# Performance work log

Measured on AMD Instinct MI355X. Metric: run time of the kernel, lower is better.

The kernel has to match this reference:

```python
import jax, jax.numpy as jnp
import numpy as np

N_NODES = 100000
N_EDGES = 1250000
IN_DIM = 128
HID_DIM = 64
OUT_DIM = 16


def setup_inputs() -> dict:
    key = jax.random.key(0)
    k1, k2, k3, k4, k5, k6, k7 = jax.random.split(key, 7)
    x = jax.random.normal(k1, (N_NODES, IN_DIM), dtype=jnp.float32)
    edge_index = jax.random.randint(k2, (2, N_EDGES), 0, N_NODES, dtype=jnp.int64)
    s = 1.0 / np.sqrt(IN_DIM)
    W1 = jax.random.uniform(k3, (IN_DIM, HID_DIM), jnp.float32, -s, s)
    b1 = jax.random.uniform(k4, (HID_DIM,), jnp.float32, -s, s)
    s2 = 1.0 / np.sqrt(HID_DIM)
    W2 = jax.random.uniform(k5, (HID_DIM, OUT_DIM), jnp.float32, -s2, s2)
    b2 = jax.random.uniform(k6, (OUT_DIM,), jnp.float32, -s2, s2)
    return {"x": x, "edge_index": edge_index, "W1": W1, "b1": b1, "W2": W2, "b2": b2}


def reference(x, edge_index, W1, b1, W2, b2):
    # GCNConv (PyG default): linear transform, add self-loops, symmetric norm,
    # gather-scatter aggregation, bias. Then relu -> linear -> log_softmax.
    N = x.shape[0]
    loop = jnp.arange(N, dtype=edge_index.dtype)
    src = jnp.concatenate([edge_index[0], loop])  # message sources
    dst = jnpp_concat = jnp.concatenate([edge_index[1], loop])  # message targets
    # degree (with self-loops) computed on destination nodes
    deg = jax.ops.segment_sum(jnp.ones_like(dst, dtype=x.dtype), dst, num_segments=N)
    deg_inv_sqrt = jnp.where(deg > 0, jax.lax.rsqrt(deg), 0.0)
    norm = deg_inv_sqrt[src] * deg_inv_sqrt[dst]  # [E+N]
    h = x @ W1  # [N, hid] -- transform before aggregation (fewer bytes moved)
    msg = h[src] * norm[:, None]  # gather: [E+N, hid]
    agg = jax.ops.segment_sum(msg, dst, num_segments=N) + b1  # scatter-add
    h = jax.nn.relu(agg)
    logits = h @ W2 + b2
    return jax.nn.log_softmax(logits, axis=-1)
```

## Files before the change

kernel.cpp:

```cpp
#include <hip/hip_runtime.h>
#include <hip/hip_bf16.h>

#define N_NODES 100000
#define N_EDGES 1250000
#define IN_DIM  128
#define HID     64
#define OUTD    16
#define ROW     64
#define NRANGE  8
#define RSIZE   12500
#define NCHUNK  128
#define CHUNK   9768
#define FILLB   (NRANGE * NCHUNK)
#define MTILE   128
#define GEMMB   ((N_NODES + MTILE - 1) / MTILE)

typedef __attribute__((ext_vector_type(8))) short  short8;
typedef __attribute__((ext_vector_type(4))) float  floatx4;
typedef __attribute__((ext_vector_type(4))) float  f32x4;
typedef __attribute__((ext_vector_type(4))) int    i32x4;

__device__ __forceinline__ unsigned short f2bf(float f) {
    unsigned u = __float_as_uint(f);
    u += 0x7fffu + ((u >> 16) & 1u);
    return (unsigned short)(u >> 16);
}
__device__ __forceinline__ unsigned pk2(float lo, float hi) {
    __hip_bfloat162 t = __float22bfloat162_rn(make_float2(lo, hi));
    return *reinterpret_cast<unsigned*>(&t);
}
__device__ __forceinline__ float bf2f_lo(unsigned u) { return __uint_as_float(u << 16); }
__device__ __forceinline__ float bf2f_hi(unsigned u) { return __uint_as_float(u & 0xffff0000u); }

__global__ __launch_bounds__(256) void zero_cursor(int* __restrict__ cursor,
                                                   unsigned* __restrict__ hb_dummy) {
    int i = blockIdx.x * 256 + threadIdx.x;
    if (i < N_NODES) cursor[i] = 0;
    if (i < 32) hb_dummy[i] = 0u;
}

__global__ __launch_bounds__(256) void fill_gemm(const float* __restrict__ x,
                                                 const float* __restrict__ W1,
                                                 const int* __restrict__ src,
                                                 const int* __restrict__ dst,
                                                 int* __restrict__ cursor,
                                                 int* __restrict__ csr,
                                                 unsigned short* __restrict__ hb) {
    __shared__ unsigned short w1t[HID][132];

    if (blockIdx.x < FILLB) {
        const int r  = blockIdx.x & 7;
        const int c  = blockIdx.x >> 3;
        const int lo = r * RSIZE;
        const int q1 = min(N_EDGES, (c + 1) * CHUNK) >> 2;
        for (int q = (c * CHUNK >> 2) + threadIdx.x; q < q1; q += 256) {
            i32x4 d4 = __builtin_nontemporal_load(((const i32x4*)dst) + q);
            i32x4 s4 = __builtin_nontemporal_load(((const i32x4*)src) + q);
#pragma unroll
            for (int u = 0; u < 4; u++) {
                int d = (u == 0) ? d4.x : (u == 1) ? d4.y : (u == 2) ? d4.z : d4.w;
                int s = (u == 0) ? s4.x : (u == 1) ? s4.y : (u == 2) ? s4.z : s4.w;
                if ((unsigned)(d - lo) < (unsigned)RSIZE) {
                    int p = atomicAdd(&cursor[d], 1);
                    if (p < ROW) csr[(size_t)d * ROW + p] = s;
                }
            }
        }
        return;
    }

    const int m0 = (blockIdx.x - FILLB) * MTILE;

    for (int q = threadIdx.x; q < IN_DIM * HID / 4; q += 256) {
        int k = q >> 4, n = (q & 15) * 4;
        float4 wq = ((const float4*)W1)[q];
        w1t[n + 0][k] = f2bf(wq.x);
        w1t[n + 1][k] = f2bf(wq.y);
        w1t[n + 2][k] = f2bf(wq.z);
        w1t[n + 3][k] = f2bf(wq.w);
    }
    __syncthreads();

    const int lane = threadIdx.x & 63;
    const int w    = threadIdx.x >> 6;
    const int mrow = lane & 15;
    const int quad = lane >> 4;
    const int rowa = min(m0 + w * 32 + mrow,      N_NODES - 1);
    const int rowb = min(m0 + w * 32 + 16 + mrow, N_NODES - 1);

    floatx4 acc[2][4] = {};
#pragma unroll
    for (int k0 = 0; k0 < IN_DIM; k0 += 32) {
        union { unsigned u[4]; short8 s; } a0, a1;
        {
            const f32x4* pa = (const f32x4*)(x + (size_t)rowa * IN_DIM + k0 + quad * 8);
            f32x4 u0 = __builtin_nontemporal_load(pa);
            f32x4 v0 = __builtin_nontemporal_load(pa + 1);
            a0.u[0] = pk2(u0.x, u0.y); a0.u[1] = pk2(u0.z, u0.w);
            a0.u[2] = pk2(v0.x, v0.y); a0.u[3] = pk2(v0.z, v0.w);
            const f32x4* pb = (const f32x4*)(x + (size_t)rowb * IN_DIM + k0 + quad * 8);
            f32x4 u1 = __builtin_nontemporal_load(pb);
            f32x4 v1 = __builtin_nontemporal_load(pb + 1);
            a1.u[0] = pk2(u1.x, u1.y); a1.u[1] = pk2(u1.z, u1.w);
            a1.u[2] = pk2(v1.x, v1.y); a1.u[3] = pk2(v1.z, v1.w);
        }
        short8 b0 = *(const short8*)&w1t[ 0 + mrow][k0 + quad * 8];
        short8 b1 = *(const short8*)&w1t[16 + mrow][k0 + quad * 8];
        short8 b2 = *(const short8*)&w1t[32 + mrow][k0 + quad * 8];
        short8 b3 = *(const short8*)&w1t[48 + mrow][k0 + quad * 8];
        acc[0][0] = __builtin_amdgcn_mfma_f32_16x16x32_bf16(a0.s, b0, acc[0][0], 0, 0, 0);
        acc[0][1] = __builtin_amdgcn_mfma_f32_16x16x32_bf16(a0.s, b1, acc[0][1], 0, 0, 0);
        acc[0][2] = __builtin_amdgcn_mfma_f32_16x16x32_bf16(a0.s, b2, acc[0][2], 0, 0, 0);
        acc[0][3] = __builtin_amdgcn_mfma_f32_16x16x32_bf16(a0.s, b3, acc[0][3], 0, 0, 0);
        acc[1][0] = __builtin_amdgcn_mfma_f32_16x16x32_bf16(a1.s, b0, acc[1][0], 0, 0, 0);
        acc[1][1] = __builtin_amdgcn_mfma_f32_16x16x32_bf16(a1.s, b1, acc[1][1], 0, 0, 0);
        acc[1][2] = __builtin_amdgcn_mfma_f32_16x16x32_bf16(a1.s, b2, acc[1][2], 0, 0, 0);
        acc[1][3] = __builtin_amdgcn_mfma_f32_16x16x32_bf16(a1.s, b3, acc[1][3], 0, 0, 0);
    }

#pragma unroll
    for (int tm = 0; tm < 2; tm++) {
#pragma unroll
        for (int reg = 0; reg < 4; reg++) {
            int m = m0 + w * 32 + tm * 16 + quad * 4 + reg;
            if (m < N_NODES) {
#pragma unroll
                for (int tn = 0; tn < 4; tn++)
                    __builtin_nontemporal_store(f2bf(acc[tm][tn][reg]),
                                                &hb[(size_t)m * HID + tn * 16 + mrow]);
            }
        }
    }
}

__global__ __launch_bounds__(256) void pull_epilogue(const unsigned short* __restrict__ hb,
                                                     const int* __restrict__ csr,
                                                     const int* __restrict__ deg,
                                                     const float* __restrict__ b1,
                                                     const float* __restrict__ W2,
                                                     const float* __restrict__ b2,
                                                     float* __restrict__ out) {
    const int i     = blockIdx.x * 4 + (threadIdx.x >> 6);
    const int lane  = threadIdx.x & 63;
    const int e_sub = lane >> 4;
    const int f4    = lane & 15;

    const int   dg  = deg[i];
    const int   cnt = min(dg, ROW - 1);
    const float di  = rsqrtf((float)dg + 1.0f);

    int   s_l = N_NODES;
    float w_l = 0.f;
    if (lane < cnt) {
        s_l = __builtin_nontemporal_load(csr + (size_t)i * ROW + lane);
        w_l = rsqrtf((float)deg[s_l] + 1.0f);
    } else if (lane == cnt) {
        s_l = i;
        w_l = di;
    }

    const uint2* hbv = (const uint2*)hb + f4;

    float ax = 0.f, ay = 0.f, az = 0.f, aw = 0.f;
    const int R = (cnt + 16) >> 4;
    for (int r = 0; r < R; ++r) {
        const int e0 = (r << 4) + e_sub;
        int   s0 = __shfl(s_l, e0,      64), s1 = __shfl(s_l, e0 + 4,  64);
        int   s2 = __shfl(s_l, e0 + 8,  64), s3 = __shfl(s_l, e0 + 12, 64);
        float w0 = __shfl(w_l, e0,      64), w1 = __shfl(w_l, e0 + 4,  64);
        float w2 = __shfl(w_l, e0 + 8,  64), w3 = __shfl(w_l, e0 + 12, 64);
        uint2 a = hbv[s0 << 4];
        uint2 b = hbv[s1 << 4];
        uint2 c = hbv[s2 << 4];
        uint2 d = hbv[s3 << 4];
        ax = fmaf(bf2f_lo(a.x), w0, ax); ay = fmaf(bf2f_hi(a.x), w0, ay);
        az = fmaf(bf2f_lo(a.y), w0, az); aw = fmaf(bf2f_hi(a.y), w0, aw);
        ax = fmaf(bf2f_lo(b.x), w1, ax); ay = fmaf(bf2f_hi(b.x), w1, ay);
        az = fmaf(bf2f_lo(b.y), w1, az); aw = fmaf(bf2f_hi(b.y), w1, aw);
        ax = fmaf(bf2f_lo(c.x), w2, ax); ay = fmaf(bf2f_hi(c.x), w2, ay);
        az = fmaf(bf2f_lo(c.y), w2, az); aw = fmaf(bf2f_hi(c.y), w2, aw);
        ax = fmaf(bf2f_lo(d.x), w3, ax); ay = fmaf(bf2f_hi(d.x), w3, ay);
        az = fmaf(bf2f_lo(d.y), w3, az); aw = fmaf(bf2f_hi(d.y), w3, aw);
    }

    ax += __shfl_xor(ax, 16, 64); ax += __shfl_xor(ax, 32, 64);
    ay += __shfl_xor(ay, 16, 64); ay += __shfl_xor(ay, 32, 64);
    az += __shfl_xor(az, 16, 64); az += __shfl_xor(az, 32, 64);
    aw += __shfl_xor(aw, 16, 64); aw += __shfl_xor(aw, 32, 64);

    float4 b1v = ((const float4*)b1)[f4];
    float v0 = fmaxf(fmaf(ax, di, b1v.x), 0.f);
    float v1 = fmaxf(fmaf(ay, di, b1v.y), 0.f);
    float v2 = fmaxf(fmaf(az, di, b1v.z), 0.f);
    float v3 = fmaxf(fmaf(aw, di, b1v.w), 0.f);

    const float4* W2v = (const float4*)W2;
    float4 w0 = W2v[(4 * f4 + 0) * 4 + e_sub];
    float4 w1 = W2v[(4 * f4 + 1) * 4 + e_sub];
    float4 w2 = W2v[(4 * f4 + 2) * 4 + e_sub];
    float4 w3 = W2v[(4 * f4 + 3) * 4 + e_sub];
    float p0 = v0 * w0.x + v1 * w1.x + v2 * w2.x + v3 * w3.x;
    float p1 = v0 * w0.y + v1 * w1.y + v2 * w2.y + v3 * w3.y;
    float p2 = v0 * w0.z + v1 * w1.z + v2 * w2.z + v3 * w3.z;
    float p3 = v0 * w0.w + v1 * w1.w + v2 * w2.w + v3 * w3.w;
#pragma unroll
    for (int d = 1; d < 16; d <<= 1) {
        p0 += __shfl_xor(p0, d, 64);
        p1 += __shfl_xor(p1, d, 64);
        p2 += __shfl_xor(p2, d, 64);
        p3 += __shfl_xor(p3, d, 64);
    }
    float4 b2v = ((const float4*)b2)[e_sub];
    float lg0 = p0 + b2v.x, lg1 = p1 + b2v.y, lg2 = p2 + b2v.z, lg3 = p3 + b2v.w;

    float m = fmaxf(fmaxf(lg0, lg1), fmaxf(lg2, lg3));
    m = fmaxf(m, __shfl_xor(m, 16, 64));
    m = fmaxf(m, __shfl_xor(m, 32, 64));
    float s = __expf(lg0 - m) + __expf(lg1 - m) + __expf(lg2 - m) + __expf(lg3 - m);
    s += __shfl_xor(s, 16, 64);
    s += __shfl_xor(s, 32, 64);
    float lse = __logf(s) + m;

    if (f4 == 0) {
        f32x4 o = {lg0 - lse, lg1 - lse, lg2 - lse, lg3 - lse};
        __builtin_nontemporal_store(o, ((f32x4*)out) + (size_t)i * 4 + e_sub);
    }
}

extern "C" void kernel_launch(void* const* d_in, const int* in_sizes, int n_in,
                              void* d_out, int out_size, void* d_ws, size_t ws_size,
                              hipStream_t stream) {
    const float* x   = (const float*)d_in[0];
    const int*   ei  = (const int*)d_in[1];
    const float* W1  = (const float*)d_in[2];
    const float* b1  = (const float*)d_in[3];
    const float* W2  = (const float*)d_in[4];
    const float* b2  = (const float*)d_in[5];
    float*       out = (float*)d_out;

    const int* src = ei;
    const int* dst = ei + N_EDGES;

    char* ws = (char*)d_ws;
    size_t off = 0;
    unsigned short* hb = (unsigned short*)(ws + off);
    off += (size_t)(N_NODES + 1) * HID * 2;
    int*   csr    = (int*)  (ws + off); off += ((size_t)N_NODES * ROW + ROW) * 4;
    int*   cursor = (int*)  (ws + off); off += (size_t)N_NODES * 4;

    zero_cursor<<<(N_NODES + 255) / 256, 256, 0, stream>>>(
        cursor, (unsigned*)(hb + (size_t)N_NODES * HID));
    fill_gemm<<<FILLB + GEMMB, 256, 0, stream>>>(x, W1, src, dst, cursor, csr, hb);
    pull_epilogue<<<N_NODES / 4, 256, 0, stream>>>(hb, csr, cursor, b1, W2, b2, out);
}
```

Before: 237.5 us.

## Fuse fill/GEMM and pull stages into one cooperative persistent kernel

Merges the CSR fill + GEMM phase and the pull/epilogue phase into one cooperative kernel with a grid-wide sync, using persistent blocks that loop over tasks and nodes. The zero-init kernel is replaced by hipMemsetAsync calls, and W2/b1/b2 loads are hoisted out of the per-node loop. The aim is to remove kernel launch gaps and per-block setup. The costs are the grid sync, a grid limited to co-resident blocks (capped at 2048), and a possible loss of load balance; a non-cooperative two-kernel fallback is kept.

```diff
diff --git a/kernel.cpp b/kernel.cpp
--- a/kernel.cpp
+++ b/kernel.cpp
@@ -1,5 +1,8 @@
 #include <hip/hip_runtime.h>
 #include <hip/hip_bf16.h>
+#include <hip/hip_cooperative_groups.h>
+
+namespace cg = cooperative_groups;
 
 #define N_NODES 100000
 #define N_EDGES 1250000
@@ -14,6 +17,7 @@
 #define FILLB   (NRANGE * NCHUNK)
 #define MTILE   128
 #define GEMMB   ((N_NODES + MTILE - 1) / MTILE)
+#define NTASK   (FILLB + GEMMB)
 
 typedef __attribute__((ext_vector_type(8))) short  short8;
 typedef __attribute__((ext_vector_type(4))) float  floatx4;
@@ -32,45 +36,38 @@
 __device__ __forceinline__ float bf2f_lo(unsigned u) { return __uint_as_float(u << 16); }
 __device__ __forceinline__ float bf2f_hi(unsigned u) { return __uint_as_float(u & 0xffff0000u); }
 
-__global__ __launch_bounds__(256) void zero_cursor(int* __restrict__ cursor,
-                                                   unsigned* __restrict__ hb_dummy) {
-    int i = blockIdx.x * 256 + threadIdx.x;
-    if (i < N_NODES) cursor[i] = 0;
-    if (i < 32) hb_dummy[i] = 0u;
-}
-
-__global__ __launch_bounds__(256) void fill_gemm(const float* __restrict__ x,
-                                                 const float* __restrict__ W1,
-                                                 const int* __restrict__ src,
-                                                 const int* __restrict__ dst,
-                                                 int* __restrict__ cursor,
-                                                 int* __restrict__ csr,
-                                                 unsigned short* __restrict__ hb) {
-    __shared__ unsigned short w1t[HID][132];
-
-    if (blockIdx.x < FILLB) {
-        const int r  = blockIdx.x & 7;
-        const int c  = blockIdx.x >> 3;
-        const int lo = r * RSIZE;
-        const int q1 = min(N_EDGES, (c + 1) * CHUNK) >> 2;
-        for (int q = (c * CHUNK >> 2) + threadIdx.x; q < q1; q += 256) {
-            i32x4 d4 = __builtin_nontemporal_load(((const i32x4*)dst) + q);
-            i32x4 s4 = __builtin_nontemporal_load(((const i32x4*)src) + q);
-#pragma unroll
-            for (int u = 0; u < 4; u++) {
-                int d = (u == 0) ? d4.x : (u == 1) ? d4.y : (u == 2) ? d4.z : d4.w;
-                int s = (u == 0) ? s4.x : (u == 1) ? s4.y : (u == 2) ? s4.z : s4.w;
-                if ((unsigned)(d - lo) < (unsigned)RSIZE) {
-                    int p = atomicAdd(&cursor[d], 1);
-                    if (p < ROW) csr[(size_t)d * ROW + p] = s;
-                }
+__device__ __forceinline__ void fill_task(int task, const int* __restrict__ src,
+                                          const int* __restrict__ dst,
+                                          int* __restrict__ cursor,
+                                          int* __restrict__ csr) {
+    const int r  = task & 7;
+    const int c  = task >> 3;
+    const int lo = r * RSIZE;
+    const int q1 = min(N_EDGES, (c + 1) * CHUNK) >> 2;
+    for (int q = (c * CHUNK >> 2) + threadIdx.x; q < q1; q += 256) {
+        i32x4 d4 = __builtin_nontemporal_load(((const i32x4*)dst) + q);
+        i32x4 s4 = __builtin_nontemporal_load(((const i32x4*)src) + q);
+#pragma unroll
+        for (int u = 0; u < 4; u++) {
+            int d = (u == 0) ? d4.x : (u == 1) ? d4.y : (u == 2) ? d4.z : d4.w;
+            int s = (u == 0) ? s4.x : (u == 1) ? s4.y : (u == 2) ? s4.z : s4.w;
+            if ((unsigned)(d - lo) < (unsigned)RSIZE) {
+                int p = atomicAdd(&cursor[d], 1);
+                if (p < ROW) csr[(size_t)d * ROW + p] = s;
             }
         }
-        return;
-    }
-
-    const int m0 = (blockIdx.x - FILLB) * MTILE;
-
+    }
+}
+
+__device__ __forceinline__ void gemm_task(int task, unsigned short (*w1t)[132],
+                                          const float* __restrict__ x,
+                                          const float* __restrict__ W1,
+                                          unsigned short* __restrict__ hb) {
+    const int m0 = (task - FILLB) * MTILE;
+    const int lane = threadIdx.x & 63;
+    const int w    = threadIdx.x >> 6;
+
+    __syncthreads();
     for (int q = threadIdx.x; q < IN_DIM * HID / 4; q += 256) {
         int k = q >> 4, n = (q & 15) * 4;
         float4 wq = ((const float4*)W1)[q];
@@ -81,8 +78,6 @@
     }
     __syncthreads();
 
-    const int lane = threadIdx.x & 63;
-    const int w    = threadIdx.x >> 6;
     const int mrow = lane & 15;
     const int quad = lane >> 4;
     const int rowa = min(m0 + w * 32 + mrow,      N_NODES - 1);
@@ -133,17 +128,16 @@
     }
 }
 
-__global__ __launch_bounds__(256) void pull_epilogue(const unsigned short* __restrict__ hb,
-                                                     const int* __restrict__ csr,
-                                                     const int* __restrict__ deg,
-                                                     const float* __restrict__ b1,
-                                                     const float* __restrict__ W2,
-                                                     const float* __restrict__ b2,
-                                                     float* __restrict__ out) {
-    const int i     = blockIdx.x * 4 + (threadIdx.x >> 6);
+__device__ __forceinline__ void pull_node(int i, const unsigned short* __restrict__ hb,
+                                          const int* __restrict__ csr,
+                                          const int* __restrict__ deg,
+                                          float4 b1v, float4 w2r0, float4 w2r1,
+                                          float4 w2r2, float4 w2r3, float4 b2v,
+                                          float* __restrict__ out) {
     const int lane  = threadIdx.x & 63;
     const int e_sub = lane >> 4;
     const int f4    = lane & 15;
+    const uint2* hbv = (const uint2*)hb + f4;
 
     const int   dg  = deg[i];
     const int   cnt = min(dg, ROW - 1);
@@ -158,8 +152,6 @@
         s_l = i;
         w_l = di;
     }
-
-    const uint2* hbv = (const uint2*)hb + f4;
 
     float ax = 0.f, ay = 0.f, az = 0.f, aw = 0.f;
     const int R = (cnt + 16) >> 4;
@@ -188,21 +180,15 @@
     az += __shfl_xor(az, 16, 64); az += __shfl_xor(az, 32, 64);
     aw += __shfl_xor(aw, 16, 64); aw += __shfl_xor(aw, 32, 64);
 
-    float4 b1v = ((const float4*)b1)[f4];
     float v0 = fmaxf(fmaf(ax, di, b1v.x), 0.f);
     float v1 = fmaxf(fmaf(ay, di, b1v.y), 0.f);
     float v2 = fmaxf(fmaf(az, di, b1v.z), 0.f);
     float v3 = fmaxf(fmaf(aw, di, b1v.w), 0.f);
 
-    const float4* W2v = (const float4*)W2;
-    float4 w0 = W2v[(4 * f4 + 0) * 4 + e_sub];
-    float4 w1 = W2v[(4 * f4 + 1) * 4 + e_sub];
-    float4 w2 = W2v[(4 * f4 + 2) * 4 + e_sub];
-    float4 w3 = W2v[(4 * f4 + 3) * 4 + e_sub];
-    float p0 = v0 * w0.x + v1 * w1.x + v2 * w2.x + v3 * w3.x;
-    float p1 = v0 * w0.y + v1 * w1.y + v2 * w2.y + v3 * w3.y;
-    float p2 = v0 * w0.z + v1 * w1.z + v2 * w2.z + v3 * w3.z;
-    float p3 = v0 * w0.w + v1 * w1.w + v2 * w2.w + v3 * w3.w;
+    float p0 = v0 * w2r0.x + v1 * w2r1.x + v2 * w2r2.x + v3 * w2r3.x;
+    float p1 = v0 * w2r0.y + v1 * w2r1.y + v2 * w2r2.y + v3 * w2r3.y;
+    float p2 = v0 * w2r0.z + v1 * w2r1.z + v2 * w2r2.z + v3 * w2r3.z;
+    float p3 = v0 * w2r0.w + v1 * w2r1.w + v2 * w2r2.w + v3 * w2r3.w;
 #pragma unroll
     for (int d = 1; d < 16; d <<= 1) {
         p0 += __shfl_xor(p0, d, 64);
@@ -210,7 +196,6 @@
         p2 += __shfl_xor(p2, d, 64);
         p3 += __shfl_xor(p3, d, 64);
     }
-    float4 b2v = ((const float4*)b2)[e_sub];
     float lg0 = p0 + b2v.x, lg1 = p1 + b2v.y, lg2 = p2 + b2v.z, lg3 = p3 + b2v.w;
 
     float m = fmaxf(fmaxf(lg0, lg1), fmaxf(lg2, lg3));
@@ -225,6 +210,78 @@
         f32x4 o = {lg0 - lse, lg1 - lse, lg2 - lse, lg3 - lse};
         __builtin_nontemporal_store(o, ((f32x4*)out) + (size_t)i * 4 + e_sub);
     }
+}
+
+__global__ __launch_bounds__(256) void fused(const float* __restrict__ x,
+                                             const float* __restrict__ W1,
+                                             const int* __restrict__ src,
+                                             const int* __restrict__ dst,
+                                             int* __restrict__ cursor,
+                                             int* __restrict__ csr,
+                                             unsigned short* __restrict__ hb,
+                                             const float* __restrict__ b1,
+                                             const float* __restrict__ W2,
+                                             const float* __restrict__ b2,
+                                             float* __restrict__ out) {
+    __shared__ unsigned short w1t[HID][132];
+
+    for (int task = blockIdx.x; task < NTASK; task += gridDim.x) {
+        if (task < FILLB) fill_task(task, src, dst, cursor, csr);
+        else              gemm_task(task, w1t, x, W1, hb);
+    }
+
+    cg::this_grid().sync();
+
+    const int lane  = threadIdx.x & 63;
+    const int w     = threadIdx.x >> 6;
+    const int e_sub = lane >> 4;
+    const int f4    = lane & 15;
+    const int* deg  = cursor;
+
+    const float4  b1v = ((const float4*)b1)[f4];
+    const float4* W2v = (const float4*)W2;
+    const float4  w2r0 = W2v[(4 * f4 + 0) * 4 + e_sub];
+    const float4  w2r1 = W2v[(4 * f4 + 1) * 4 + e_sub];
+    const float4  w2r2 = W2v[(4 * f4 + 2) * 4 + e_sub];
+    const float4  w2r3 = W2v[(4 * f4 + 3) * 4 + e_sub];
+    const float4  b2v = ((const float4*)b2)[e_sub];
+
+    const int nw = gridDim.x * 4;
+    for (int i = blockIdx.x * 4 + w; i < N_NODES; i += nw)
+        pull_node(i, hb, csr, deg, b1v, w2r0, w2r1, w2r2, w2r3, b2v, out);
+}
+
+__global__ __launch_bounds__(256) void fill_gemm_k(const float* __restrict__ x,
+                                                   const float* __restrict__ W1,
+                                                   const int* __restrict__ src,
+                                                   const int* __restrict__ dst,
+                                                   int* __restrict__ cursor,
+                                                   int* __restrict__ csr,
+                                                   unsigned short* __restrict__ hb) {
+    __shared__ unsigned short w1t[HID][132];
+    if (blockIdx.x < FILLB) fill_task(blockIdx.x, src, dst, cursor, csr);
+    else                    gemm_task(blockIdx.x, w1t, x, W1, hb);
+}
+
+__global__ __launch_bounds__(256) void pull_k(const unsigned short* __restrict__ hb,
+                                              const int* __restrict__ csr,
+                                              const int* __restrict__ deg,
+                                              const float* __restrict__ b1,
+                                              const float* __restrict__ W2,
+                                              const float* __restrict__ b2,
+                                              float* __restrict__ out) {
+    const int lane  = threadIdx.x & 63;
+    const int e_sub = lane >> 4;
+    const int f4    = lane & 15;
+    const float4  b1v = ((const float4*)b1)[f4];
+    const float4* W2v = (const float4*)W2;
+    const float4  w2r0 = W2v[(4 * f4 + 0) * 4 + e_sub];
+    const float4  w2r1 = W2v[(4 * f4 + 1) * 4 + e_sub];
+    const float4  w2r2 = W2v[(4 * f4 + 2) * 4 + e_sub];
+    const float4  w2r3 = W2v[(4 * f4 + 3) * 4 + e_sub];
+    const float4  b2v = ((const float4*)b2)[e_sub];
+    const int i = blockIdx.x * 4 + (threadIdx.x >> 6);
+    pull_node(i, hb, csr, deg, b1v, w2r0, w2r1, w2r2, w2r3, b2v, out);
 }
 
 extern "C" void kernel_launch(void* const* d_in, const int* in_sizes, int n_in,
@@ -248,8 +305,37 @@
     int*   csr    = (int*)  (ws + off); off += ((size_t)N_NODES * ROW + ROW) * 4;
     int*   cursor = (int*)  (ws + off); off += (size_t)N_NODES * 4;
 
-    zero_cursor<<<(N_NODES + 255) / 256, 256, 0, stream>>>(
-        cursor, (unsigned*)(hb + (size_t)N_NODES * HID));
-    fill_gemm<<<FILLB + GEMMB, 256, 0, stream>>>(x, W1, src, dst, cursor, csr, hb);
-    pull_epilogue<<<N_NODES / 4, 256, 0, stream>>>(hb, csr, cursor, b1, W2, b2, out);
-}
+    static int coopGrid = -2;
+    if (coopGrid == -2) {
+        int bpc = 0, ncu = 256;
+        hipDeviceProp_t prop;
+        if (hipGetDeviceProperties(&prop, 0) == hipSuccess) ncu = prop.multiProcessorCount;
+        if (hipOccupancyMaxActiveBlocksPerMultiprocessor(&bpc, (const void*)fused, 256, 0)
+                == hipSuccess && bpc >= 1) {
+            int g = bpc * ncu;
+            if (g > 2048) g = 2048;
+            g &= ~7;
+            coopGrid = (g >= 8) ? g : -1;
+        } else {
+            coopGrid = -1;
+        }
+    }
+
+    hipMemsetAsync(cursor, 0, (size_t)N_NODES * 4, stream);
+    hipMemsetAsync(hb + (size_t)N_NODES * HID, 0, HID * sizeof(unsigned short), stream);
+
+    bool done = false;
+    if (coopGrid > 0) {
+        void* args[] = {(void*)&x, (void*)&W1, (void*)&src, (void*)&dst,
+                        (void*)&cursor, (void*)&csr, (void*)&hb,
+                        (void*)&b1, (void*)&W2, (void*)&b2, (void*)&out};
+        hipError_t e = hipLaunchCooperativeKernel((const void*)fused, dim3(coopGrid),
+                                                  dim3(256), args, 0, stream);
+        if (e == hipSuccess) done = true;
+        else coopGrid = -1;
+    }
+    if (!done) {
+        fill_gemm_k<<<FILLB + GEMMB, 256, 0, stream>>>(x, W1, src, dst, cursor, csr, hb);
+        pull_k<<<N_NODES / 4, 256, 0, stream>>>(hb, csr, cursor, b1, W2, b2, out);
+    }
+}
```

New measurement: 376.8 us. 1.59x slower.

## Process four nodes per wavefront in pull epilogue and batch fill atomics

Applied to the files above, without the earlier changes.

The pull/epilogue kernel now gives each wavefront four destination nodes and interleaves their gathers, so more independent loads are in flight per wave and the W2/b1/b2 loads are shared. The fill phase issues its four atomics before the dependent CSR stores and uses twice as many, smaller chunks. The zeroing kernel is replaced by hipMemsetAsync, and padding source lanes now point at node 0 with weight 0 instead of a zeroed dummy row. This trades more registers and less wave-level parallelism in the epilogue for memory-level parallelism.

```diff
diff --git a/kernel.cpp b/kernel.cpp
--- a/kernel.cpp
+++ b/kernel.cpp
@@ -9,11 +9,12 @@
 #define ROW     64
 #define NRANGE  8
 #define RSIZE   12500
-#define NCHUNK  128
-#define CHUNK   9768
+#define NCHUNK  256
+#define CHUNK   4888
 #define FILLB   (NRANGE * NCHUNK)
 #define MTILE   128
 #define GEMMB   ((N_NODES + MTILE - 1) / MTILE)
+#define NPW     4
 
 typedef __attribute__((ext_vector_type(8))) short  short8;
 typedef __attribute__((ext_vector_type(4))) float  floatx4;
@@ -31,13 +32,6 @@
 }
 __device__ __forceinline__ float bf2f_lo(unsigned u) { return __uint_as_float(u << 16); }
 __device__ __forceinline__ float bf2f_hi(unsigned u) { return __uint_as_float(u & 0xffff0000u); }
-
-__global__ __launch_bounds__(256) void zero_cursor(int* __restrict__ cursor,
-                                                   unsigned* __restrict__ hb_dummy) {
-    int i = blockIdx.x * 256 + threadIdx.x;
-    if (i < N_NODES) cursor[i] = 0;
-    if (i < 32) hb_dummy[i] = 0u;
-}
 
 __global__ __launch_bounds__(256) void fill_gemm(const float* __restrict__ x,
                                                  const float* __restrict__ W1,
@@ -56,15 +50,19 @@
         for (int q = (c * CHUNK >> 2) + threadIdx.x; q < q1; q += 256) {
             i32x4 d4 = __builtin_nontemporal_load(((const i32x4*)dst) + q);
             i32x4 s4 = __builtin_nontemporal_load(((const i32x4*)src) + q);
-#pragma unroll
-            for (int u = 0; u < 4; u++) {
-                int d = (u == 0) ? d4.x : (u == 1) ? d4.y : (u == 2) ? d4.z : d4.w;
-                int s = (u == 0) ? s4.x : (u == 1) ? s4.y : (u == 2) ? s4.z : s4.w;
-                if ((unsigned)(d - lo) < (unsigned)RSIZE) {
-                    int p = atomicAdd(&cursor[d], 1);
-                    if (p < ROW) csr[(size_t)d * ROW + p] = s;
-                }
-            }
+            int p0 = 0, p1 = 0, p2 = 0, p3 = 0;
+            const bool k0 = (unsigned)(d4.x - lo) < (unsigned)RSIZE;
+            const bool k1 = (unsigned)(d4.y - lo) < (unsigned)RSIZE;
+            const bool k2 = (unsigned)(d4.z - lo) < (unsigned)RSIZE;
+            const bool k3 = (unsigned)(d4.w - lo) < (unsigned)RSIZE;
+            if (k0) p0 = atomicAdd(&cursor[d4.x], 1);
+            if (k1) p1 = atomicAdd(&cursor[d4.y], 1);
+            if (k2) p2 = atomicAdd(&cursor[d4.z], 1);
+            if (k3) p3 = atomicAdd(&cursor[d4.w], 1);
+            if (k0 && p0 < ROW) csr[(size_t)d4.x * ROW + p0] = s4.x;
+            if (k1 && p1 < ROW) csr[(size_t)d4.y * ROW + p1] = s4.y;
+            if (k2 && p2 < ROW) csr[(size_t)d4.z * ROW + p2] = s4.z;
+            if (k3 && p3 < ROW) csr[(size_t)d4.w * ROW + p3] = s4.w;
         }
         return;
     }
@@ -140,90 +138,143 @@
                                                      const float* __restrict__ W2,
                                                      const float* __restrict__ b2,
                                                      float* __restrict__ out) {
-    const int i     = blockIdx.x * 4 + (threadIdx.x >> 6);
     const int lane  = threadIdx.x & 63;
     const int e_sub = lane >> 4;
     const int f4    = lane & 15;
-
-    const int   dg  = deg[i];
-    const int   cnt = min(dg, ROW - 1);
-    const float di  = rsqrtf((float)dg + 1.0f);
-
-    int   s_l = N_NODES;
-    float w_l = 0.f;
-    if (lane < cnt) {
-        s_l = __builtin_nontemporal_load(csr + (size_t)i * ROW + lane);
-        w_l = rsqrtf((float)deg[s_l] + 1.0f);
-    } else if (lane == cnt) {
-        s_l = i;
-        w_l = di;
+    const int base  = blockIdx.x * (4 * NPW) + (threadIdx.x >> 6) * NPW;
+
+    int   dg[NPW], cnt[NPW];
+    float di[NPW];
+#pragma unroll
+    for (int n = 0; n < NPW; n++) {
+        dg[n]  = deg[base + n];
+        cnt[n] = min(dg[n], ROW - 1);
+        di[n]  = rsqrtf((float)dg[n] + 1.0f);
+    }
+
+    int sv[NPW];
+#pragma unroll
+    for (int n = 0; n < NPW; n++) {
+        sv[n] = 0;
+        if (lane < cnt[n])
+            sv[n] = __builtin_nontemporal_load(csr + (size_t)(base + n) * ROW + lane);
+    }
+    float wv[NPW];
+#pragma unroll
+    for (int n = 0; n < NPW; n++) {
+        wv[n] = 0.f;
+        if (lane < cnt[n])       wv[n] = rsqrtf((float)deg[sv[n]] + 1.0f);
+        else if (lane == cnt[n]) { sv[n] = base + n; wv[n] = di[n]; }
     }
 
     const uint2* hbv = (const uint2*)hb + f4;
 
-    float ax = 0.f, ay = 0.f, az = 0.f, aw = 0.f;
-    const int R = (cnt + 16) >> 4;
+    float ax[NPW], ay[NPW], az[NPW], aw[NPW];
+    int   Rn[NPW];
+    int   R = 0;
+#pragma unroll
+    for (int n = 0; n < NPW; n++) {
+        ax[n] = ay[n] = az[n] = aw[n] = 0.f;
+        Rn[n] = (cnt[n] + 16) >> 4;
+        R = max(R, Rn[n]);
+    }
+
     for (int r = 0; r < R; ++r) {
         const int e0 = (r << 4) + e_sub;
-        int   s0 = __shfl(s_l, e0,      64), s1 = __shfl(s_l, e0 + 4,  64);
-        int   s2 = __shfl(s_l, e0 + 8,  64), s3 = __shfl(s_l, e0 + 12, 64);
-        float w0 = __shfl(w_l, e0,      64), w1 = __shfl(w_l, e0 + 4,  64);
-        float w2 = __shfl(w_l, e0 + 8,  64), w3 = __shfl(w_l, e0 + 12, 64);
-        uint2 a = hbv[s0 << 4];
-        uint2 b = hbv[s1 << 4];
-        uint2 c = hbv[s2 << 4];
-        uint2 d = hbv[s3 << 4];
-        ax = fmaf(bf2f_lo(a.x), w0, ax); ay = fmaf(bf2f_hi(a.x), w0, ay);
-        az = fmaf(bf2f_lo(a.y), w0, az); aw = fmaf(bf2f_hi(a.y), w0, aw);
-        ax = fmaf(bf2f_lo(b.x), w1, ax); ay = fmaf(bf2f_hi(b.x), w1, ay);
-        az = fmaf(bf2f_lo(b.y), w1, az); aw = fmaf(bf2f_hi(b.y), w1, aw);
-        ax = fmaf(bf2f_lo(c.x), w2, ax); ay = fmaf(bf2f_hi(c.x), w2, ay);
-        az = fmaf(bf2f_lo(c.y), w2, az); aw = fmaf(bf2f_hi(c.y), w2, aw);
-        ax = fmaf(bf2f_lo(d.x), w3, ax); ay = fmaf(bf2f_hi(d.x), w3, ay);
-        az = fmaf(bf2f_lo(d.y), w3, az); aw = fmaf(bf2f_hi(d.y), w3, aw);
-    }
-
-    ax += __shfl_xor(ax, 16, 64); ax += __shfl_xor(ax, 32, 64);
-    ay += __shfl_xor(ay, 16, 64); ay += __shfl_xor(ay, 32, 64);
-    az += __shfl_xor(az, 16, 64); az += __shfl_xor(az, 32, 64);
-    aw += __shfl_xor(aw, 16, 64); aw += __shfl_xor(aw, 32, 64);
-
-    float4 b1v = ((const float4*)b1)[f4];
-    float v0 = fmaxf(fmaf(ax, di, b1v.x), 0.f);
-    float v1 = fmaxf(fmaf(ay, di, b1v.y), 0.f);
-    float v2 = fmaxf(fmaf(az, di, b1v.z), 0.f);
-    float v3 = fmaxf(fmaf(aw, di, b1v.w), 0.f);
+#pragma unroll
+        for (int n = 0; n < NPW; n++) {
+            if (r < Rn[n]) {
+                int   s0 = __shfl(sv[n], e0,      64), s1 = __shfl(sv[n], e0 + 4,  64);
+                int   s2 = __shfl(sv[n], e0 + 8,  64), s3 = __shfl(sv[n], e0 + 12, 64);
+                float w0 = __shfl(wv[n], e0,      64), w1 = __shfl(wv[n], e0 + 4,  64);
+                float w2 = __shfl(wv[n], e0 + 8,  64), w3 = __shfl(wv[n], e0 + 12, 64);
+                uint2 a = hbv[s0 << 4];
+                uint2 b = hbv[s1 << 4];
+                uint2 c = hbv[s2 << 4];
+                uint2 d = hbv[s3 << 4];
+                ax[n] = fmaf(bf2f_lo(a.x), w0, ax[n]); ay[n] = fmaf(bf2f_hi(a.x), w0, ay[n]);
+                az[n] = fmaf(bf2f_lo(a.y), w0, az[n]); aw[n] = fmaf(bf2f_hi(a.y), w0, aw[n]);
+                ax[n] = fmaf(bf2f_lo(b.x), w1, ax[n]); ay[n] = fmaf(bf2f_hi(b.x), w1, ay[n]);
+                az[n] = fmaf(bf2f_lo(b.y), w1, az[n]); aw[n] = fmaf(bf2f_hi(b.y), w1, aw[n]);
+                ax[n] = fmaf(bf2f_lo(c.x), w2, ax[n]); ay[n] = fmaf(bf2f_hi(c.x), w2, ay[n]);
+                az[n] = fmaf(bf2f_lo(c.y), w2, az[n]); aw[n] = fmaf(bf2f_hi(c.y), w2, aw[n]);
+                ax[n] = fmaf(bf2f_lo(d.x), w3, ax[n]); ay[n] = fmaf(bf2f_hi(d.x), w3, ay[n]);
+                az[n] = fmaf(bf2f_lo(d.y), w3, az[n]); aw[n] = fmaf(bf2f_hi(d.y), w3, aw[n]);
+            }
+        }
+    }
+
+#pragma unroll
+    for (int n = 0; n < NPW; n++) {
+        ax[n] += __shfl_xor(ax[n], 16, 64); ay[n] += __shfl_xor(ay[n], 16, 64);
+        az[n] += __shfl_xor(az[n], 16, 64); aw[n] += __shfl_xor(aw[n], 16, 64);
+    }
+#pragma unroll
+    for (int n = 0; n < NPW; n++) {
+        ax[n] += __shfl_xor(ax[n], 32, 64); ay[n] += __shfl_xor(ay[n], 32, 64);
+        az[n] += __shfl_xor(az[n], 32, 64); aw[n] += __shfl_xor(aw[n], 32, 64);
+    }
+
+    const float4 b1v = ((const float4*)b1)[f4];
+    float4 v[NPW];
+#pragma unroll
+    for (int n = 0; n < NPW; n++) {
+        v[n].x = fmaxf(fmaf(ax[n], di[n], b1v.x), 0.f);
+        v[n].y = fmaxf(fmaf(ay[n], di[n], b1v.y), 0.f);
+        v[n].z = fmaxf(fmaf(az[n], di[n], b1v.z), 0.f);
+        v[n].w = fmaxf(fmaf(aw[n], di[n], b1v.w), 0.f);
+    }
 
     const float4* W2v = (const float4*)W2;
-    float4 w0 = W2v[(4 * f4 + 0) * 4 + e_sub];
-    float4 w1 = W2v[(4 * f4 + 1) * 4 + e_sub];
-    float4 w2 = W2v[(4 * f4 + 2) * 4 + e_sub];
-    float4 w3 = W2v[(4 * f4 + 3) * 4 + e_sub];
-    float p0 = v0 * w0.x + v1 * w1.x + v2 * w2.x + v3 * w3.x;
-    float p1 = v0 * w0.y + v1 * w1.y + v2 * w2.y + v3 * w3.y;
-    float p2 = v0 * w0.z + v1 * w1.z + v2 * w2.z + v3 * w3.z;
-    float p3 = v0 * w0.w + v1 * w1.w + v2 * w2.w + v3 * w3.w;
+    const float4 w2r0 = W2v[(4 * f4 + 0) * 4 + e_sub];
+    const float4 w2r1 = W2v[(4 * f4 + 1) * 4 + e_sub];
+    const float4 w2r2 = W2v[(4 * f4 + 2) * 4 + e_sub];
+    const float4 w2r3 = W2v[(4 * f4 + 3) * 4 + e_sub];
+    float4 p[NPW];
+#pragma unroll
+    for (int n = 0; n < NPW; n++) {
+        p[n].x = v[n].x * w2r0.x + v[n].y * w2r1.x + v[n].z * w2r2.x + v[n].w * w2r3.x;
+        p[n].y = v[n].x * w2r0.y + v[n].y * w2r1.y + v[n].z * w2r2.y + v[n].w * w2r3.y;
+        p[n].z = v[n].x * w2r0.z + v[n].y * w2r1.z + v[n].z * w2r2.z + v[n].w * w2r3.z;
+        p[n].w = v[n].x * w2r0.w + v[n].y * w2r1.w + v[n].z * w2r2.w + v[n].w * w2r3.w;
+    }
 #pragma unroll
     for (int d = 1; d < 16; d <<= 1) {
-        p0 += __shfl_xor(p0, d, 64);
-        p1 += __shfl_xor(p1, d, 64);
-        p2 += __shfl_xor(p2, d, 64);
-        p3 += __shfl_xor(p3, d, 64);
-    }
-    float4 b2v = ((const float4*)b2)[e_sub];
-    float lg0 = p0 + b2v.x, lg1 = p1 + b2v.y, lg2 = p2 + b2v.z, lg3 = p3 + b2v.w;
-
-    float m = fmaxf(fmaxf(lg0, lg1), fmaxf(lg2, lg3));
-    m = fmaxf(m, __shfl_xor(m, 16, 64));
-    m = fmaxf(m, __shfl_xor(m, 32, 64));
-    float s = __expf(lg0 - m) + __expf(lg1 - m) + __expf(lg2 - m) + __expf(lg3 - m);
-    s += __shfl_xor(s, 16, 64);
-    s += __shfl_xor(s, 32, 64);
-    float lse = __logf(s) + m;
+#pragma unroll
+        for (int n = 0; n < NPW; n++) {
+            p[n].x += __shfl_xor(p[n].x, d, 64);
+            p[n].y += __shfl_xor(p[n].y, d, 64);
+            p[n].z += __shfl_xor(p[n].z, d, 64);
+            p[n].w += __shfl_xor(p[n].w, d, 64);
+        }
+    }
+    const float4 b2v = ((const float4*)b2)[e_sub];
+    float m[NPW], s[NPW];
+#pragma unroll
+    for (int n = 0; n < NPW; n++) {
+        p[n].x += b2v.x; p[n].y += b2v.y; p[n].z += b2v.z; p[n].w += b2v.w;
+        m[n] = fmaxf(fmaxf(p[n].x, p[n].y), fmaxf(p[n].z, p[n].w));
+    }
+#pragma unroll
+    for (int n = 0; n < NPW; n++) m[n] = fmaxf(m[n], __shfl_xor(m[n], 16, 64));
+#pragma unroll
+    for (int n = 0; n < NPW; n++) m[n] = fmaxf(m[n], __shfl_xor(m[n], 32, 64));
+#pragma unroll
+    for (int n = 0; n < NPW; n++)
+        s[n] = __expf(p[n].x - m[n]) + __expf(p[n].y - m[n]) +
+               __expf(p[n].z - m[n]) + __expf(p[n].w - m[n]);
+#pragma unroll
+    for (int n = 0; n < NPW; n++) s[n] += __shfl_xor(s[n], 16, 64);
+#pragma unroll
+    for (int n = 0; n < NPW; n++) s[n] += __shfl_xor(s[n], 32, 64);
 
     if (f4 == 0) {
-        f32x4 o = {lg0 - lse, lg1 - lse, lg2 - lse, lg3 - lse};
-        __builtin_nontemporal_store(o, ((f32x4*)out) + (size_t)i * 4 + e_sub);
+#pragma unroll
+        for (int n = 0; n < NPW; n++) {
+            float lse = __logf(s[n]) + m[n];
+            f32x4 o = {p[n].x - lse, p[n].y - lse, p[n].z - lse, p[n].w - lse};
+            __builtin_nontemporal_store(o, ((f32x4*)out) + (size_t)(base + n) * 4 + e_sub);
+        }
     }
 }
 
@@ -244,12 +295,12 @@
     char* ws = (char*)d_ws;
     size_t off = 0;
     unsigned short* hb = (unsigned short*)(ws + off);
-    off += (size_t)(N_NODES + 1) * HID * 2;
+    off += (size_t)N_NODES * HID * 2;
     int*   csr    = (int*)  (ws + off); off += ((size_t)N_NODES * ROW + ROW) * 4;
     int*   cursor = (int*)  (ws + off); off += (size_t)N_NODES * 4;
 
-    zero_cursor<<<(N_NODES + 255) / 256, 256, 0, stream>>>(
-        cursor, (unsigned*)(hb + (size_t)N_NODES * HID));
+    hipMemsetAsync(cursor, 0, (size_t)N_NODES * 4, stream);
+
     fill_gemm<<<FILLB + GEMMB, 256, 0, stream>>>(x, W1, src, dst, cursor, csr, hb);
-    pull_epilogue<<<N_NODES / 4, 256, 0, stream>>>(hb, csr, cursor, b1, W2, b2, out);
-}
+    pull_epilogue<<<N_NODES / (4 * NPW), 256, 0, stream>>>(hb, csr, cursor, b1, W2, b2, out);
+}
```

Measured after the change: 216.2 us. -9.0%, faster.
